# Optimization experiments

Hardware: AMD Instinct MI355X
Metric: run time of the kernel (lower is better)

Reference implementation:

```python
import jax, jax.numpy as jnp
import numpy as np

EPS = 1e-5

def setup_inputs() -> dict:
    key = jax.random.key(0)
    k1, k2 = jax.random.split(key)
    B, S, F = 16, 8192, 256
    x = jax.random.normal(k1, (B, S, F), dtype=jnp.float32)
    change_points = (jax.random.uniform(k2, (B, S)) < 0.001).astype(jnp.int32)
    affine_weight = jnp.ones((F,), dtype=jnp.float32)
    affine_bias = jnp.zeros((F,), dtype=jnp.float32)
    return {"x": x, "affine_weight": affine_weight, "affine_bias": affine_bias,
            "change_points": change_points}


def _segment_normalize(x, affine_weight, affine_bias, change_points):
    # x: [B, S, F]; change_points: [B, S] int
    B, S, F = x.shape
    # Torch loop: a boundary fires at position i (i >= 1) if ANY batch has a cp.
    ind = (jnp.sum(change_points, axis=0) > 0).astype(jnp.int32)  # [S]
    ind = ind.at[0].set(0)  # loop starts at i=1; position 0 never splits
    seg_id = jnp.cumsum(ind)  # [S], segment index shared across batch

    xt = jnp.swapaxes(x, 0, 1)  # [S, B, F]
    ones = jnp.ones((S,), dtype=x.dtype)
    counts = jax.ops.segment_sum(ones, seg_id, num_segments=S)  # [S]
    ssum = jax.ops.segment_sum(xt, seg_id, num_segments=S)      # [S, B, F]
    ssq = jax.ops.segment_sum(xt * xt, seg_id, num_segments=S)  # [S, B, F]
    cnt = jnp.maximum(counts, 1.0)[:, None, None]
    mean = ssum / cnt                                   # per-segment mean (biased var)
    var = jnp.maximum(ssq / cnt - mean * mean, 0.0)
    std = jnp.sqrt(var + EPS)
    # stats are .detach()ed in the original
    mean_t = jax.lax.stop_gradient(mean)[seg_id]  # gather back to [S, B, F]
    std_t = jax.lax.stop_gradient(std)[seg_id]
    xn = (xt - mean_t) / std_t
    xn = jnp.swapaxes(xn, 0, 1)  # [B, S, F]
    xn = xn * affine_weight + affine_bias
    return xn


def reference(x, affine_weight, affine_bias, change_points):
    return _segment_normalize(x, affine_weight, affine_bias, change_points)
```

## Files before the change

kernel.cpp:

```cpp
#include <hip/hip_runtime.h>

#define BSZ 16
#define SSZ 8192
#define FSZ 256
#define EPSV 1e-5f

__global__ void cp_reduce_kernel(const int* __restrict__ cp, int* __restrict__ ind) {
    int s = blockIdx.x * blockDim.x + threadIdx.x;
    if (s >= SSZ) return;
    int a = 0;
#pragma unroll
    for (int b = 0; b < BSZ; ++b) a |= cp[b * SSZ + s];
    ind[s] = (s == 0) ? 0 : (a != 0 ? 1 : 0);
}

__global__ __launch_bounds__(1024) void scan_kernel(const int* __restrict__ ind,
                                                    int* __restrict__ seg_starts,
                                                    int* __restrict__ nseg_out) {
    __shared__ int lds[1024];
    int t = threadIdx.x;
    int vals[8];
    int tot = 0;
#pragma unroll
    for (int i = 0; i < 8; ++i) {
        int s = t * 8 + i;
        int v = ind[s];
        vals[i] = v;
        tot += v;
    }
    lds[t] = tot;
    __syncthreads();
    for (int off = 1; off < 1024; off <<= 1) {
        int a = lds[t];
        int b = (t >= off) ? lds[t - off] : 0;
        __syncthreads();
        lds[t] = a + b;
        __syncthreads();
    }
    int run = lds[t] - tot;
#pragma unroll
    for (int i = 0; i < 8; ++i) {
        int s = t * 8 + i;
        if (vals[i]) {
            run += 1;
            seg_starts[run] = s;
        }
    }
    if (t == 0) seg_starts[0] = 0;
    if (t == 1023) nseg_out[0] = lds[1023] + 1;
}

__global__ __launch_bounds__(256) void segnorm_kernel(const float4* __restrict__ x4,
                                                      const float4* __restrict__ w4p,
                                                      const float4* __restrict__ b4p,
                                                      const int* __restrict__ seg_starts,
                                                      const int* __restrict__ nseg_p,
                                                      float4* __restrict__ out4) {
    __shared__ float4 p_sum[4][64];
    __shared__ float4 p_ssq[4][64];
    const int nseg = nseg_p[0];
    const int nitems = nseg * BSZ;
    const int lane = threadIdx.x & 63;
    const int wave = threadIdx.x >> 6;
    const float4 w = w4p[lane];
    const float4 bb = b4p[lane];

    for (int item = blockIdx.x; item < nitems; item += gridDim.x) {
        const int seg = item >> 4;
        const int b = item & 15;
        const int start = seg_starts[seg];
        const int end = (seg + 1 < nseg) ? seg_starts[seg + 1] : SSZ;

        const float4* px = x4 + (size_t)b * SSZ * 64 + lane;

        float4 sum = make_float4(0.f, 0.f, 0.f, 0.f);
        float4 ssq = make_float4(0.f, 0.f, 0.f, 0.f);
        for (int s = start + wave; s < end; s += 4) {
            float4 v = px[(size_t)s * 64];
            sum.x += v.x; sum.y += v.y; sum.z += v.z; sum.w += v.w;
            ssq.x += v.x * v.x; ssq.y += v.y * v.y; ssq.z += v.z * v.z; ssq.w += v.w * v.w;
        }
        p_sum[wave][lane] = sum;
        p_ssq[wave][lane] = ssq;
        __syncthreads();

        float4 ts = make_float4(0.f, 0.f, 0.f, 0.f);
        float4 tq = make_float4(0.f, 0.f, 0.f, 0.f);
#pragma unroll
        for (int wv = 0; wv < 4; ++wv) {
            float4 a = p_sum[wv][lane];
            float4 q = p_ssq[wv][lane];
            ts.x += a.x; ts.y += a.y; ts.z += a.z; ts.w += a.w;
            tq.x += q.x; tq.y += q.y; tq.z += q.z; tq.w += q.w;
        }
        __syncthreads();

        const float cnt = (float)(end - start);
        const float rc = 1.0f / cnt;
        float4 mean, rstd;
        mean.x = ts.x * rc; mean.y = ts.y * rc; mean.z = ts.z * rc; mean.w = ts.w * rc;
        float vx = fmaxf(tq.x * rc - mean.x * mean.x, 0.f);
        float vy = fmaxf(tq.y * rc - mean.y * mean.y, 0.f);
        float vz = fmaxf(tq.z * rc - mean.z * mean.z, 0.f);
        float vw = fmaxf(tq.w * rc - mean.w * mean.w, 0.f);
        rstd.x = 1.0f / sqrtf(vx + EPSV);
        rstd.y = 1.0f / sqrtf(vy + EPSV);
        rstd.z = 1.0f / sqrtf(vz + EPSV);
        rstd.w = 1.0f / sqrtf(vw + EPSV);

        float4* po = out4 + (size_t)b * SSZ * 64 + lane;
        for (int s = start + wave; s < end; s += 4) {
            float4 v = px[(size_t)s * 64];
            float4 o;
            o.x = (v.x - mean.x) * rstd.x * w.x + bb.x;
            o.y = (v.y - mean.y) * rstd.y * w.y + bb.y;
            o.z = (v.z - mean.z) * rstd.z * w.z + bb.z;
            o.w = (v.w - mean.w) * rstd.w * w.w + bb.w;
            po[(size_t)s * 64] = o;
        }
    }
}

extern "C" void kernel_launch(void* const* d_in, const int* in_sizes, int n_in,
                              void* d_out, int out_size, void* d_ws, size_t ws_size,
                              hipStream_t stream) {
    const float* x = (const float*)d_in[0];
    const float* w = (const float*)d_in[1];
    const float* bias = (const float*)d_in[2];
    const int* cp = (const int*)d_in[3];

    int* wsi = (int*)d_ws;
    int* nseg = wsi;
    int* seg_starts = wsi + 64;
    int* ind = wsi + 64 + SSZ;

    cp_reduce_kernel<<<(SSZ + 255) / 256, 256, 0, stream>>>(cp, ind);
    scan_kernel<<<1, 1024, 0, stream>>>(ind, seg_starts, nseg);
    segnorm_kernel<<<2048, 256, 0, stream>>>((const float4*)x, (const float4*)w,
                                             (const float4*)bias, seg_starts, nseg,
                                             (float4*)d_out);
}
```

Measured before the change: 102.9 us.

## Split segment normalization into chunked atomic stats pass and separate normalize pass

```diff
diff --git a/kernel.cpp b/kernel.cpp
--- a/kernel.cpp
+++ b/kernel.cpp
@@ -3,7 +3,9 @@
 #define BSZ 16
 #define SSZ 8192
 #define FSZ 256
+#define F4  64
 #define EPSV 1e-5f
+#define SEGCAP 256
 
 __global__ void cp_reduce_kernel(const int* __restrict__ cp, int* __restrict__ ind) {
     int s = blockIdx.x * blockDim.x + threadIdx.x;
@@ -16,18 +18,14 @@
 
 __global__ __launch_bounds__(1024) void scan_kernel(const int* __restrict__ ind,
                                                     int* __restrict__ seg_starts,
+                                                    int* __restrict__ seg_id,
                                                     int* __restrict__ nseg_out) {
     __shared__ int lds[1024];
     int t = threadIdx.x;
     int vals[8];
     int tot = 0;
 #pragma unroll
-    for (int i = 0; i < 8; ++i) {
-        int s = t * 8 + i;
-        int v = ind[s];
-        vals[i] = v;
-        tot += v;
-    }
+    for (int i = 0; i < 8; ++i) { int v = ind[t * 8 + i]; vals[i] = v; tot += v; }
     lds[t] = tot;
     __syncthreads();
     for (int off = 1; off < 1024; off <<= 1) {
@@ -41,83 +39,124 @@
 #pragma unroll
     for (int i = 0; i < 8; ++i) {
         int s = t * 8 + i;
-        if (vals[i]) {
-            run += 1;
-            seg_starts[run] = s;
-        }
+        run += vals[i];
+        if (vals[i]) seg_starts[run] = s;
+        seg_id[s] = run;
     }
     if (t == 0) seg_starts[0] = 0;
     if (t == 1023) nseg_out[0] = lds[1023] + 1;
 }
 
-__global__ __launch_bounds__(256) void segnorm_kernel(const float4* __restrict__ x4,
-                                                      const float4* __restrict__ w4p,
-                                                      const float4* __restrict__ b4p,
-                                                      const int* __restrict__ seg_starts,
-                                                      const int* __restrict__ nseg_p,
-                                                      float4* __restrict__ out4) {
-    __shared__ float4 p_sum[4][64];
-    __shared__ float4 p_ssq[4][64];
-    const int nseg = nseg_p[0];
-    const int nitems = nseg * BSZ;
+__global__ void zero_kernel(float4* __restrict__ sum4, float4* __restrict__ ssq4,
+                            const int* __restrict__ nseg_p) {
+    int n4 = nseg_p[0] * BSZ * F4;
+    int stride = gridDim.x * blockDim.x;
+    float4 z = make_float4(0.f, 0.f, 0.f, 0.f);
+    for (int i = blockIdx.x * blockDim.x + threadIdx.x; i < n4; i += stride) {
+        sum4[i] = z;
+        ssq4[i] = z;
+    }
+}
+
+__device__ inline void flushacc(float* __restrict__ as, float* __restrict__ aq,
+                                int seg, int b, int lane,
+                                const float4& s4, const float4& q4) {
+    int base = ((seg * BSZ + b) << 8) + (lane << 2);
+    atomicAdd(as + base + 0, s4.x);
+    atomicAdd(as + base + 1, s4.y);
+    atomicAdd(as + base + 2, s4.z);
+    atomicAdd(as + base + 3, s4.w);
+    atomicAdd(aq + base + 0, q4.x);
+    atomicAdd(aq + base + 1, q4.y);
+    atomicAdd(aq + base + 2, q4.z);
+    atomicAdd(aq + base + 3, q4.w);
+}
+
+__global__ __launch_bounds__(256) void stats_kernel(const float4* __restrict__ x4,
+                                                    const int* __restrict__ seg_id,
+                                                    float* __restrict__ acc_sum,
+                                                    float* __restrict__ acc_ssq) {
+    const int c = blockIdx.x;
+    const int b = c >> 7;
+    const int s0 = (c & 127) << 6;
     const int lane = threadIdx.x & 63;
     const int wave = threadIdx.x >> 6;
-    const float4 w = w4p[lane];
-    const float4 bb = b4p[lane];
+    const float4* px = x4 + ((size_t)b * SSZ + s0) * F4 + lane;
 
-    for (int item = blockIdx.x; item < nitems; item += gridDim.x) {
-        const int seg = item >> 4;
-        const int b = item & 15;
-        const int start = seg_starts[seg];
-        const int end = (seg + 1 < nseg) ? seg_starts[seg + 1] : SSZ;
+    float4 sum = make_float4(0.f, 0.f, 0.f, 0.f);
+    float4 ssq = make_float4(0.f, 0.f, 0.f, 0.f);
+    int cur = seg_id[s0 + wave];
 
-        const float4* px = x4 + (size_t)b * SSZ * 64 + lane;
+#pragma unroll
+    for (int h = 0; h < 2; ++h) {
+        float4 v[8];
+        int sid[8];
+#pragma unroll
+        for (int r = 0; r < 8; ++r) {
+            int srow = wave + 4 * (h * 8 + r);
+            v[r] = px[(size_t)srow * F4];
+            sid[r] = seg_id[s0 + srow];
+        }
+#pragma unroll
+        for (int r = 0; r < 8; ++r) {
+            if (sid[r] != cur) {
+                flushacc(acc_sum, acc_ssq, cur, b, lane, sum, ssq);
+                sum = make_float4(0.f, 0.f, 0.f, 0.f);
+                ssq = make_float4(0.f, 0.f, 0.f, 0.f);
+                cur = sid[r];
+            }
+            sum.x += v[r].x; sum.y += v[r].y; sum.z += v[r].z; sum.w += v[r].w;
+            ssq.x += v[r].x * v[r].x; ssq.y += v[r].y * v[r].y;
+            ssq.z += v[r].z * v[r].z; ssq.w += v[r].w * v[r].w;
+        }
+    }
+    flushacc(acc_sum, acc_ssq, cur, b, lane, sum, ssq);
+}
 
-        float4 sum = make_float4(0.f, 0.f, 0.f, 0.f);
-        float4 ssq = make_float4(0.f, 0.f, 0.f, 0.f);
-        for (int s = start + wave; s < end; s += 4) {
-            float4 v = px[(size_t)s * 64];
-            sum.x += v.x; sum.y += v.y; sum.z += v.z; sum.w += v.w;
-            ssq.x += v.x * v.x; ssq.y += v.y * v.y; ssq.z += v.z * v.z; ssq.w += v.w * v.w;
-        }
-        p_sum[wave][lane] = sum;
-        p_ssq[wave][lane] = ssq;
-        __syncthreads();
+__global__ void finalize_kernel(float* __restrict__ acc_sum, float* __restrict__ acc_ssq,
+                                const int* __restrict__ seg_starts,
+                                const int* __restrict__ nseg_p) {
+    int nseg = nseg_p[0];
+    int total = nseg * BSZ * FSZ;
+    int stride = gridDim.x * blockDim.x;
+    for (int i = blockIdx.x * blockDim.x + threadIdx.x; i < total; i += stride) {
+        int seg = i >> 12;
+        int st = seg_starts[seg];
+        int en = (seg + 1 < nseg) ? seg_starts[seg + 1] : SSZ;
+        float rc = 1.0f / (float)(en - st);
+        float sm = acc_sum[i] * rc;
+        float vv = fmaxf(acc_ssq[i] * rc - sm * sm, 0.0f);
+        acc_sum[i] = sm;
+        acc_ssq[i] = 1.0f / sqrtf(vv + EPSV);
+    }
+}
 
-        float4 ts = make_float4(0.f, 0.f, 0.f, 0.f);
-        float4 tq = make_float4(0.f, 0.f, 0.f, 0.f);
+__global__ __launch_bounds__(256) void norm_kernel(const float4* __restrict__ x4,
+                                                   const float4* __restrict__ w4p,
+                                                   const float4* __restrict__ b4p,
+                                                   const int* __restrict__ seg_id,
+                                                   const float4* __restrict__ mean4,
+                                                   const float4* __restrict__ rstd4,
+                                                   float4* __restrict__ out4) {
+    int tid = blockIdx.x * blockDim.x + threadIdx.x;
+    int f4 = tid & 63;
+    int s = tid >> 6;
+    float4 w = w4p[f4];
+    float4 bb = b4p[f4];
+    int seg = seg_id[s];
+    size_t xi = (size_t)s * F4 + f4;
+    int mi = (seg * BSZ) * F4 + f4;
 #pragma unroll
-        for (int wv = 0; wv < 4; ++wv) {
-            float4 a = p_sum[wv][lane];
-            float4 q = p_ssq[wv][lane];
-            ts.x += a.x; ts.y += a.y; ts.z += a.z; ts.w += a.w;
-            tq.x += q.x; tq.y += q.y; tq.z += q.z; tq.w += q.w;
-        }
-        __syncthreads();
-
-        const float cnt = (float)(end - start);
-        const float rc = 1.0f / cnt;
-        float4 mean, rstd;
-        mean.x = ts.x * rc; mean.y = ts.y * rc; mean.z = ts.z * rc; mean.w = ts.w * rc;
-        float vx = fmaxf(tq.x * rc - mean.x * mean.x, 0.f);
-        float vy = fmaxf(tq.y * rc - mean.y * mean.y, 0.f);
-        float vz = fmaxf(tq.z * rc - mean.z * mean.z, 0.f);
-        float vw = fmaxf(tq.w * rc - mean.w * mean.w, 0.f);
-        rstd.x = 1.0f / sqrtf(vx + EPSV);
-        rstd.y = 1.0f / sqrtf(vy + EPSV);
-        rstd.z = 1.0f / sqrtf(vz + EPSV);
-        rstd.w = 1.0f / sqrtf(vw + EPSV);
-
-        float4* po = out4 + (size_t)b * SSZ * 64 + lane;
-        for (int s = start + wave; s < end; s += 4) {
-            float4 v = px[(size_t)s * 64];
-            float4 o;
-            o.x = (v.x - mean.x) * rstd.x * w.x + bb.x;
-            o.y = (v.y - mean.y) * rstd.y * w.y + bb.y;
-            o.z = (v.z - mean.z) * rstd.z * w.z + bb.z;
-            o.w = (v.w - mean.w) * rstd.w * w.w + bb.w;
-            po[(size_t)s * 64] = o;
-        }
+    for (int b = 0; b < BSZ; ++b) {
+        float4 v = x4[xi + (size_t)b * SSZ * F4];
+        float4 m = mean4[mi + b * F4];
+        float4 r = rstd4[mi + b * F4];
+        float4 o;
+        o.x = (v.x - m.x) * r.x * w.x + bb.x;
+        o.y = (v.y - m.y) * r.y * w.y + bb.y;
+        o.z = (v.z - m.z) * r.z * w.z + bb.z;
+        o.w = (v.w - m.w) * r.w * w.w + bb.w;
+        out4[xi + (size_t)b * SSZ * F4] = o;
     }
 }
 
@@ -129,14 +168,21 @@
     const float* bias = (const float*)d_in[2];
     const int* cp = (const int*)d_in[3];
 
-    int* wsi = (int*)d_ws;
-    int* nseg = wsi;
-    int* seg_starts = wsi + 64;
-    int* ind = wsi + 64 + SSZ;
+    char* ws = (char*)d_ws;
+    int* nseg = (int*)ws;
+    int* seg_starts = (int*)(ws + 256);
+    int* seg_id = (int*)(ws + 256 + 32768);
+    int* ind = (int*)(ws + 256 + 65536);
+    float* acc_sum = (float*)(ws + 131072);
+    float* acc_ssq = acc_sum + SEGCAP * BSZ * FSZ;
 
     cp_reduce_kernel<<<(SSZ + 255) / 256, 256, 0, stream>>>(cp, ind);
-    scan_kernel<<<1, 1024, 0, stream>>>(ind, seg_starts, nseg);
-    segnorm_kernel<<<2048, 256, 0, stream>>>((const float4*)x, (const float4*)w,
-                                             (const float4*)bias, seg_starts, nseg,
-                                             (float4*)d_out);
+    scan_kernel<<<1, 1024, 0, stream>>>(ind, seg_starts, seg_id, nseg);
+    zero_kernel<<<256, 256, 0, stream>>>((float4*)acc_sum, (float4*)acc_ssq, nseg);
+    stats_kernel<<<2048, 256, 0, stream>>>((const float4*)x, seg_id, acc_sum, acc_ssq);
+    finalize_kernel<<<256, 256, 0, stream>>>(acc_sum, acc_ssq, seg_starts, nseg);
+    norm_kernel<<<2048, 256, 0, stream>>>((const float4*)x, (const float4*)w,
+                                          (const float4*)bias, seg_id,
+                                          (const float4*)acc_sum, (const float4*)acc_ssq,
+                                          (float4*)d_out);
 }
```

Result: slower. 279.6 us (+171.7%).

## Sort segments by length and split feature halves for balanced segment normalization

Applied to the files above, without the earlier changes.

```diff
diff --git a/kernel.cpp b/kernel.cpp
--- a/kernel.cpp
+++ b/kernel.cpp
@@ -2,8 +2,12 @@
 
 #define BSZ 16
 #define SSZ 8192
-#define FSZ 256
+#define F4  64
 #define EPSV 1e-5f
+#define SEGCAP 256
+#define NBLK 2048
+
+typedef float f32x4 __attribute__((ext_vector_type(4)));
 
 __global__ void cp_reduce_kernel(const int* __restrict__ cp, int* __restrict__ ind) {
     int s = blockIdx.x * blockDim.x + threadIdx.x;
@@ -14,20 +18,18 @@
     ind[s] = (s == 0) ? 0 : (a != 0 ? 1 : 0);
 }
 
-__global__ __launch_bounds__(1024) void scan_kernel(const int* __restrict__ ind,
-                                                    int* __restrict__ seg_starts,
-                                                    int* __restrict__ nseg_out) {
+__global__ __launch_bounds__(1024) void scan_sort_kernel(const int* __restrict__ ind,
+                                                         int* __restrict__ sorted_st,
+                                                         int* __restrict__ sorted_en,
+                                                         int* __restrict__ meta) {
     __shared__ int lds[1024];
-    int t = threadIdx.x;
+    __shared__ int sstart[SEGCAP];
+    __shared__ int snseg;
+    const int t = threadIdx.x;
     int vals[8];
     int tot = 0;
 #pragma unroll
-    for (int i = 0; i < 8; ++i) {
-        int s = t * 8 + i;
-        int v = ind[s];
-        vals[i] = v;
-        tot += v;
-    }
+    for (int i = 0; i < 8; ++i) { int v = ind[t * 8 + i]; vals[i] = v; tot += v; }
     lds[t] = tot;
     __syncthreads();
     for (int off = 1; off < 1024; off <<= 1) {
@@ -40,83 +42,90 @@
     int run = lds[t] - tot;
 #pragma unroll
     for (int i = 0; i < 8; ++i) {
-        int s = t * 8 + i;
-        if (vals[i]) {
-            run += 1;
-            seg_starts[run] = s;
+        run += vals[i];
+        if (vals[i] && run < SEGCAP) sstart[run] = t * 8 + i;
+    }
+    if (t == 0) sstart[0] = 0;
+    if (t == 1023) { int n = lds[1023] + 1; snseg = n < SEGCAP ? n : SEGCAP; }
+    __syncthreads();
+
+    const int nseg = snseg;
+    if (t < nseg) {
+        const int st = sstart[t];
+        const int en = (t + 1 < nseg) ? sstart[t + 1] : SSZ;
+        const int len = en - st;
+        int rank = 0;
+        for (int j = 0; j < nseg; ++j) {
+            const int stj = sstart[j];
+            const int enj = (j + 1 < nseg) ? sstart[j + 1] : SSZ;
+            const int lj = enj - stj;
+            rank += (lj > len) || (lj == len && j < t);
         }
+        sorted_st[rank] = st;
+        sorted_en[rank] = en;
     }
-    if (t == 0) seg_starts[0] = 0;
-    if (t == 1023) nseg_out[0] = lds[1023] + 1;
+    if (t == 0) meta[0] = nseg;
 }
 
-__global__ __launch_bounds__(256) void segnorm_kernel(const float4* __restrict__ x4,
-                                                      const float4* __restrict__ w4p,
-                                                      const float4* __restrict__ b4p,
-                                                      const int* __restrict__ seg_starts,
-                                                      const int* __restrict__ nseg_p,
-                                                      float4* __restrict__ out4) {
-    __shared__ float4 p_sum[4][64];
-    __shared__ float4 p_ssq[4][64];
-    const int nseg = nseg_p[0];
-    const int nitems = nseg * BSZ;
-    const int lane = threadIdx.x & 63;
-    const int wave = threadIdx.x >> 6;
-    const float4 w = w4p[lane];
-    const float4 bb = b4p[lane];
+__global__ __launch_bounds__(256) void segnorm_kernel(const f32x4* __restrict__ x4,
+                                                      const f32x4* __restrict__ w4p,
+                                                      const f32x4* __restrict__ b4p,
+                                                      const int* __restrict__ sorted_st,
+                                                      const int* __restrict__ sorted_en,
+                                                      const int* __restrict__ meta,
+                                                      f32x4* __restrict__ out4) {
+    __shared__ f32x4 lsum[8][32];
+    __shared__ f32x4 lssq[8][32];
+    __shared__ f32x4 lmean[32];
+    __shared__ f32x4 lrstd[32];
+    const int nitems = meta[0] * 32;
+    const int col = threadIdx.x & 31;
+    const int rg = threadIdx.x >> 5;
 
-    for (int item = blockIdx.x; item < nitems; item += gridDim.x) {
-        const int seg = item >> 4;
-        const int b = item & 15;
-        const int start = seg_starts[seg];
-        const int end = (seg + 1 < nseg) ? seg_starts[seg + 1] : SSZ;
+    for (int item = blockIdx.x; item < nitems; item += NBLK) {
+        const int k = item >> 5;
+        const int b = (item >> 1) & 15;
+        const int fh = item & 1;
+        const int st = sorted_st[k];
+        const int en = sorted_en[k];
+        const f32x4* px = x4 + (size_t)b * SSZ * F4 + fh * 32 + col;
 
-        const float4* px = x4 + (size_t)b * SSZ * 64 + lane;
-
-        float4 sum = make_float4(0.f, 0.f, 0.f, 0.f);
-        float4 ssq = make_float4(0.f, 0.f, 0.f, 0.f);
-        for (int s = start + wave; s < end; s += 4) {
-            float4 v = px[(size_t)s * 64];
-            sum.x += v.x; sum.y += v.y; sum.z += v.z; sum.w += v.w;
-            ssq.x += v.x * v.x; ssq.y += v.y * v.y; ssq.z += v.z * v.z; ssq.w += v.w * v.w;
+        f32x4 sum = {0.f, 0.f, 0.f, 0.f};
+        f32x4 ssq = {0.f, 0.f, 0.f, 0.f};
+        for (int s = st + rg; s < en; s += 8) {
+            f32x4 v = px[(size_t)s * F4];
+            sum += v;
+            ssq += v * v;
         }
-        p_sum[wave][lane] = sum;
-        p_ssq[wave][lane] = ssq;
+        lsum[rg][col] = sum;
+        lssq[rg][col] = ssq;
         __syncthreads();
-
-        float4 ts = make_float4(0.f, 0.f, 0.f, 0.f);
-        float4 tq = make_float4(0.f, 0.f, 0.f, 0.f);
+        if (threadIdx.x < 32) {
+            f32x4 S = {0.f, 0.f, 0.f, 0.f};
+            f32x4 Q = {0.f, 0.f, 0.f, 0.f};
 #pragma unroll
-        for (int wv = 0; wv < 4; ++wv) {
-            float4 a = p_sum[wv][lane];
-            float4 q = p_ssq[wv][lane];
-            ts.x += a.x; ts.y += a.y; ts.z += a.z; ts.w += a.w;
-            tq.x += q.x; tq.y += q.y; tq.z += q.z; tq.w += q.w;
+            for (int r = 0; r < 8; ++r) { S += lsum[r][threadIdx.x]; Q += lssq[r][threadIdx.x]; }
+            const float rc = 1.0f / (float)(en - st);
+            f32x4 m = S * rc;
+            f32x4 var = Q * rc - m * m;
+            f32x4 rr;
+            rr.x = 1.0f / sqrtf(fmaxf(var.x, 0.f) + EPSV);
+            rr.y = 1.0f / sqrtf(fmaxf(var.y, 0.f) + EPSV);
+            rr.z = 1.0f / sqrtf(fmaxf(var.z, 0.f) + EPSV);
+            rr.w = 1.0f / sqrtf(fmaxf(var.w, 0.f) + EPSV);
+            lmean[threadIdx.x] = m;
+            lrstd[threadIdx.x] = rr;
         }
         __syncthreads();
-
-        const float cnt = (float)(end - start);
-        const float rc = 1.0f / cnt;
-        float4 mean, rstd;
-        mean.x = ts.x * rc; mean.y = ts.y * rc; mean.z = ts.z * rc; mean.w = ts.w * rc;
-        float vx = fmaxf(tq.x * rc - mean.x * mean.x, 0.f);
-        float vy = fmaxf(tq.y * rc - mean.y * mean.y, 0.f);
-        float vz = fmaxf(tq.z * rc - mean.z * mean.z, 0.f);
-        float vw = fmaxf(tq.w * rc - mean.w * mean.w, 0.f);
-        rstd.x = 1.0f / sqrtf(vx + EPSV);
-        rstd.y = 1.0f / sqrtf(vy + EPSV);
-        rstd.z = 1.0f / sqrtf(vz + EPSV);
-        rstd.w = 1.0f / sqrtf(vw + EPSV);
-
-        float4* po = out4 + (size_t)b * SSZ * 64 + lane;
-        for (int s = start + wave; s < end; s += 4) {
-            float4 v = px[(size_t)s * 64];
-            float4 o;
-            o.x = (v.x - mean.x) * rstd.x * w.x + bb.x;
-            o.y = (v.y - mean.y) * rstd.y * w.y + bb.y;
-            o.z = (v.z - mean.z) * rstd.z * w.z + bb.z;
-            o.w = (v.w - mean.w) * rstd.w * w.w + bb.w;
-            po[(size_t)s * 64] = o;
+        const f32x4 m = lmean[col];
+        const f32x4 r = lrstd[col];
+        const f32x4 w = w4p[fh * 32 + col];
+        const f32x4 bb = b4p[fh * 32 + col];
+        f32x4* po = out4 + (size_t)b * SSZ * F4 + fh * 32 + col;
+        for (int s = st + rg; s < en; s += 8) {
+            f32x4 v = px[(size_t)s * F4];
+            f32x4 o = (v - m) * r * w + bb;
+            __builtin_nontemporal_store(o, &po[(size_t)s * F4]);
         }
     }
 }
@@ -124,19 +133,19 @@
 extern "C" void kernel_launch(void* const* d_in, const int* in_sizes, int n_in,
                               void* d_out, int out_size, void* d_ws, size_t ws_size,
                               hipStream_t stream) {
-    const float* x = (const float*)d_in[0];
-    const float* w = (const float*)d_in[1];
-    const float* bias = (const float*)d_in[2];
+    const f32x4* x = (const f32x4*)d_in[0];
+    const f32x4* w = (const f32x4*)d_in[1];
+    const f32x4* bias = (const f32x4*)d_in[2];
     const int* cp = (const int*)d_in[3];
 
-    int* wsi = (int*)d_ws;
-    int* nseg = wsi;
-    int* seg_starts = wsi + 64;
-    int* ind = wsi + 64 + SSZ;
+    char* ws = (char*)d_ws;
+    int* meta = (int*)ws;
+    int* sorted_st = (int*)(ws + 1024);
+    int* sorted_en = (int*)(ws + 4096);
+    int* ind = (int*)(ws + 8192);
 
     cp_reduce_kernel<<<(SSZ + 255) / 256, 256, 0, stream>>>(cp, ind);
-    scan_kernel<<<1, 1024, 0, stream>>>(ind, seg_starts, nseg);
-    segnorm_kernel<<<2048, 256, 0, stream>>>((const float4*)x, (const float4*)w,
-                                             (const float4*)bias, seg_starts, nseg,
-                                             (float4*)d_out);
+    scan_sort_kernel<<<1, 1024, 0, stream>>>(ind, sorted_st, sorted_en, meta);
+    segnorm_kernel<<<NBLK, 256, 0, stream>>>(x, w, bias, sorted_st, sorted_en, meta,
+                                             (f32x4*)d_out);
 }
```

Result: faster. 100.6 us (-2.3%).
